# Optimization experiments

Hardware: AMD Instinct MI355X
Metric: run time of the kernel (lower is better)

The kernel has to match this reference:

```python
import jax, jax.numpy as jnp
import numpy as np
from jax import lax

CANTOR_DEPTH = 8
VOCAB, D = 100000, 128


def setup_inputs() -> dict:
    key = jax.random.key(0)
    pentachora = jax.random.normal(key, (VOCAB, 5, D), dtype=jnp.float32)
    return {"pentachora": pentachora}


def _cantor_positions(V):
    # V: [N, 5, D]
    dt = V.dtype
    diff = V[:, :, None, :] - V[:, None, :, :]          # [N,5,5,D]
    dist_sq = jnp.sum(diff * diff, axis=-1)             # [N,5,5]
    N = V.shape[0]

    # Batched 6x6 Cayley-Menger matrix
    M = jnp.zeros((N, 6, 6), dtype=dt)
    M = M.at[:, 0, 1:].set(1.0)
    M = M.at[:, 1:, 0].set(1.0)
    M = M.at[:, 1:, 1:].set(dist_sq)
    det = jnp.linalg.det(M)                              # [N]
    volume = jnp.sqrt(jnp.clip(-det / 9216.0, 0.0))

    # Edge statistics over the 10 unique edges (torch .std() uses ddof=1)
    iu, ju = np.triu_indices(5, k=1)
    edge_lengths = jnp.sqrt(dist_sq[:, iu, ju])          # [N,10]
    mean_edge = jnp.mean(edge_lengths, axis=-1)
    std_edge = jnp.std(edge_lengths, axis=-1, ddof=1)

    # Vertex spread from centroid (ddof=1)
    centroid = jnp.mean(V, axis=1, keepdims=True)        # [N,1,D]
    cdist = jnp.linalg.norm(V - centroid, axis=-1)       # [N,5]
    spread = jnp.std(cdist, axis=-1, ddof=1)

    volume_norm = jax.nn.sigmoid(volume * 10.0)
    edge_ratio = jax.nn.sigmoid(std_edge / (mean_edge + 1e-6))
    spread_norm = jax.nn.sigmoid(spread)

    seed = jnp.clip(volume_norm * 0.4 + edge_ratio * 0.3 + spread_norm * 0.3,
                    1e-6, 1.0 - 1e-6)
    drift = (volume_norm + edge_ratio + spread_norm) * 0.01

    def step(carry, factor):
        x, cv = carry
        x_scaled = x * 3.0
        digit = jnp.floor(x_scaled)                      # x>0 so floor==trunc
        x_frac = x_scaled - digit
        cv = cv + (digit == 2.0).astype(dt) * factor
        x = jnp.clip(x_frac + drift, 1e-6, 1.0 - 1e-6)
        return (x, cv), None

    factors = (0.5 ** jnp.arange(1, CANTOR_DEPTH + 1)).astype(dt)
    (_, cantor_val), _ = lax.scan(step, (seed, jnp.zeros_like(seed)), factors)
    return jnp.clip(cantor_val, 0.0, 1.0)                # [N]


def reference(pentachora):
    return _cantor_positions(pentachora)
```

## Files before the change

### kernel.cpp

```cpp
#include <hip/hip_runtime.h>
#include <math.h>


__global__ __launch_bounds__(256) void fingerprint_kernel(
    const float* __restrict__ pent, float* __restrict__ out, int nItems)
{
    const int tid  = threadIdx.x;
    const int wave = tid >> 6;
    const int lane = tid & 63;
    const int grp  = lane >> 3;
    const int s    = lane & 7;

    long item  = (long)blockIdx.x * 32 + (long)wave * 8 + grp;
    long itemC = item < nItems ? item : (long)nItems - 1;

    const float4* __restrict__ p =
        reinterpret_cast<const float4*>(pent + itemC * 640L);

    float4 f[5][4];
#pragma unroll
    for (int v = 0; v < 5; ++v)
#pragma unroll
        for (int j = 0; j < 4; ++j)
            f[v][j] = p[v * 32 + j * 8 + s];

    const float* fp = reinterpret_cast<const float*>(f);

    double g[15];
#pragma unroll
    for (int q = 0; q < 15; ++q) g[q] = 0.0;

#pragma unroll
    for (int t = 0; t < 16; ++t) {
        double a[5];
#pragma unroll
        for (int v = 0; v < 5; ++v)
            a[v] = (double)fp[v * 16 + t];
        int q = 0;
#pragma unroll
        for (int i = 0; i < 5; ++i)
#pragma unroll
            for (int j = i; j < 5; ++j) {
                g[q] = fma(a[i], a[j], g[q]);
                ++q;
            }
    }

#pragma unroll
    for (int m = 1; m <= 4; m <<= 1)
#pragma unroll
        for (int q = 0; q < 15; ++q) g[q] += __shfl_xor(g[q], m, 64);


    double G[5][5];
    {
        int q = 0;
#pragma unroll
        for (int i = 0; i < 5; ++i)
#pragma unroll
            for (int j = i; j < 5; ++j) {
                G[i][j] = g[q];
                G[j][i] = g[q];
                ++q;
            }
    }

    double S[5], T = 0.0;
#pragma unroll
    for (int i = 0; i < 5; ++i) {
        S[i] = G[i][0] + G[i][1] + G[i][2] + G[i][3] + G[i][4];
        T += S[i];
    }

    double d2[10];
    {
        int q = 0;
#pragma unroll
        for (int i = 0; i < 5; ++i)
#pragma unroll
            for (int j = i + 1; j < 5; ++j) {
                d2[q] = fma(-2.0, G[i][j], G[i][i] + G[j][j]);
                ++q;
            }
    }

    double W[4][4];
#pragma unroll
    for (int pi = 0; pi < 4; ++pi)
#pragma unroll
        for (int qi = 0; qi < 4; ++qi)
            W[pi][qi] = G[pi + 1][qi + 1] - G[0][qi + 1] - G[pi + 1][0] + G[0][0];

    double det = 1.0;
#pragma unroll
    for (int k = 0; k < 4; ++k) {
        double pv = W[k][k];
        det *= pv;
        double inv = (pv != 0.0) ? 1.0 / pv : 0.0;
#pragma unroll
        for (int r = k + 1; r < 4; ++r) {
            double fac = W[r][k] * inv;
#pragma unroll
            for (int c = k + 1; c < 4; ++c)
                W[r][c] = fma(-fac, W[k][c], W[r][c]);
        }
    }

    double v2 = det / 576.0;
    double volume = (v2 > 0.0) ? sqrt(v2) : 0.0;

    double e[10], se = 0.0;
#pragma unroll
    for (int q = 0; q < 10; ++q) { e[q] = sqrt(d2[q]); se += e[q]; }
    double meanE = se * 0.1;
    double ve = 0.0;
#pragma unroll
    for (int q = 0; q < 10; ++q) { double d = e[q] - meanE; ve = fma(d, d, ve); }
    double stdE = sqrt(ve / 9.0);

    double cd[5], scd = 0.0;
#pragma unroll
    for (int v = 0; v < 5; ++v) {
        double c2 = fma(-0.4, S[v], G[v][v]) + 0.04 * T;
        cd[v] = (c2 > 0.0) ? sqrt(c2) : 0.0;
        scd += cd[v];
    }
    double meanC = scd * 0.2;
    double vc = 0.0;
#pragma unroll
    for (int v = 0; v < 5; ++v) { double d = cd[v] - meanC; vc = fma(d, d, vc); }
    double spread = sqrt(vc * 0.25);

    double vn = 1.0 / (1.0 + exp(-10.0 * volume));
    double er = 1.0 / (1.0 + exp(-(stdE / (meanE + 1e-6))));
    double sn = 1.0 / (1.0 + exp(-spread));

    double seed = 0.4 * vn + 0.3 * er + 0.3 * sn;
    seed = fmin(fmax(seed, 1e-6), 1.0 - 1e-6);
    double drift = (vn + er + sn) * 0.01;

    double x = seed, cv = 0.0, factor = 0.5;
#pragma unroll
    for (int k = 0; k < 8; ++k) {
        double xs = x * 3.0;
        double dg = floor(xs);
        double fr = xs - dg;
        cv += (dg == 2.0) ? factor : 0.0;
        factor *= 0.5;
        x = fmin(fmax(fr + drift, 1e-6), 1.0 - 1e-6);
    }
    cv = fmin(fmax(cv, 0.0), 1.0);

    if (s == 0 && item < nItems)
        out[item] = (float)cv;
}

extern "C" void kernel_launch(void* const* d_in, const int* in_sizes, int n_in,
                              void* d_out, int out_size, void* d_ws, size_t ws_size,
                              hipStream_t stream) {
    const float* pent = (const float*)d_in[0];
    float* out = (float*)d_out;
    int nItems = in_sizes[0] / 640;
    int blocks = (nItems + 31) / 32;
    hipLaunchKernelGGL(fingerprint_kernel, dim3(blocks), dim3(256), 0, stream,
                       pent, out, nItems);
}
```

Before: 49.36 us.

## Compact per-item epilogue into one wave via LDS handoff of Gram sums

After the shuffle reduction, each 8-lane group writes its 15 reduced Gram entries to shared memory. The first 32 threads then each run the scalar double-precision epilogue (distances, determinant, sigmoids, Cantor loop) for one item, instead of all 256 lanes computing it redundantly. This cuts the redundant FP64 work to one wave per block, at the cost of a block barrier and LDS traffic. The launch bounds also gain a minimum-blocks hint, which may constrain register allocation.

```diff
diff --git a/kernel.cpp b/kernel.cpp
--- a/kernel.cpp
+++ b/kernel.cpp
@@ -2,9 +2,15 @@
 #include <math.h>
 
 
-__global__ __launch_bounds__(256) void fingerprint_kernel(
+__device__ __forceinline__ constexpr int gidx(int i, int j) {
+    return i * 5 - i * (i - 1) / 2 + (j - i);
+}
+
+__global__ __launch_bounds__(256, 4) void fingerprint_kernel(
     const float* __restrict__ pent, float* __restrict__ out, int nItems)
 {
+    __shared__ double lds_g[32][15];
+
     const int tid  = threadIdx.x;
     const int wave = tid >> 6;
     const int lane = tid & 63;
@@ -51,108 +57,128 @@
 #pragma unroll
         for (int q = 0; q < 15; ++q) g[q] += __shfl_xor(g[q], m, 64);
 
+    if (s == 0) {
+        const int slot = wave * 8 + grp;
+#pragma unroll
+        for (int q = 0; q < 15; ++q) lds_g[slot][q] = g[q];
+    }
+    __syncthreads();
 
-    double G[5][5];
-    {
-        int q = 0;
+    if (tid < 32) {
+        const long item2 = (long)blockIdx.x * 32 + tid;
+
+        double h[15];
 #pragma unroll
-        for (int i = 0; i < 5; ++i)
+        for (int q = 0; q < 15; ++q) h[q] = lds_g[tid][q];
+
+        double e[10];
+        double se = 0.0;
+        {
+            int q = 0;
 #pragma unroll
-            for (int j = i; j < 5; ++j) {
-                G[i][j] = g[q];
-                G[j][i] = g[q];
-                ++q;
+            for (int i = 0; i < 5; ++i)
+#pragma unroll
+                for (int j = i + 1; j < 5; ++j) {
+                    double d2 = fma(-2.0, h[gidx(i, j)],
+                                    h[gidx(i, i)] + h[gidx(j, j)]);
+                    e[q] = sqrt(d2);
+                    se += e[q];
+                    ++q;
+                }
+        }
+        double meanE = se * 0.1;
+        double ve = 0.0;
+#pragma unroll
+        for (int q = 0; q < 10; ++q) {
+            double d = e[q] - meanE;
+            ve = fma(d, d, ve);
+        }
+        double stdE = sqrt(ve / 9.0);
+
+        double S[5], T = 0.0;
+#pragma unroll
+        for (int i = 0; i < 5; ++i) {
+            double si = 0.0;
+#pragma unroll
+            for (int j = 0; j < 5; ++j) {
+                int a = i < j ? i : j;
+                int b = i < j ? j : i;
+                si += h[gidx(a, b)];
             }
+            S[i] = si;
+            T += si;
+        }
+
+        double scd = 0.0, cd[5];
+#pragma unroll
+        for (int v = 0; v < 5; ++v) {
+            double c2 = fma(-0.4, S[v], h[gidx(v, v)]) + 0.04 * T;
+            cd[v] = (c2 > 0.0) ? sqrt(c2) : 0.0;
+            scd += cd[v];
+        }
+        double meanC = scd * 0.2;
+        double vc = 0.0;
+#pragma unroll
+        for (int v = 0; v < 5; ++v) {
+            double d = cd[v] - meanC;
+            vc = fma(d, d, vc);
+        }
+        double spread = sqrt(vc * 0.25);
+
+        double W[4][4];
+#pragma unroll
+        for (int pi = 0; pi < 4; ++pi)
+#pragma unroll
+            for (int qi = 0; qi < 4; ++qi) {
+                int a0 = 0, b0 = qi + 1;
+                int a1 = 0, b1 = pi + 1;
+                int lo = (pi < qi ? pi : qi) + 1;
+                int hi = (pi < qi ? qi : pi) + 1;
+                W[pi][qi] = h[gidx(lo, hi)] - h[gidx(a0, b0)]
+                          - h[gidx(a1, b1)] + h[gidx(0, 0)];
+            }
+
+        double det = 1.0;
+#pragma unroll
+        for (int k = 0; k < 4; ++k) {
+            double pv = W[k][k];
+            det *= pv;
+            double inv = (pv != 0.0) ? 1.0 / pv : 0.0;
+#pragma unroll
+            for (int r = k + 1; r < 4; ++r) {
+                double fac = W[r][k] * inv;
+#pragma unroll
+                for (int c = k + 1; c < 4; ++c)
+                    W[r][c] = fma(-fac, W[k][c], W[r][c]);
+            }
+        }
+
+        double v2 = det / 576.0;
+        double volume = (v2 > 0.0) ? sqrt(v2) : 0.0;
+
+        double vn = 1.0 / (1.0 + exp(-10.0 * volume));
+        double er = 1.0 / (1.0 + exp(-(stdE / (meanE + 1e-6))));
+        double sn = 1.0 / (1.0 + exp(-spread));
+
+        double seed = 0.4 * vn + 0.3 * er + 0.3 * sn;
+        seed = fmin(fmax(seed, 1e-6), 1.0 - 1e-6);
+        double drift = (vn + er + sn) * 0.01;
+
+        double x = seed, cv = 0.0, factor = 0.5;
+#pragma unroll
+        for (int k = 0; k < 8; ++k) {
+            double xs = x * 3.0;
+            double dg = floor(xs);
+            double fr = xs - dg;
+            cv += (dg == 2.0) ? factor : 0.0;
+            factor *= 0.5;
+            x = fmin(fmax(fr + drift, 1e-6), 1.0 - 1e-6);
+        }
+        cv = fmin(fmax(cv, 0.0), 1.0);
+
+        if (item2 < nItems)
+            out[item2] = (float)cv;
     }
-
-    double S[5], T = 0.0;
-#pragma unroll
-    for (int i = 0; i < 5; ++i) {
-        S[i] = G[i][0] + G[i][1] + G[i][2] + G[i][3] + G[i][4];
-        T += S[i];
-    }
-
-    double d2[10];
-    {
-        int q = 0;
-#pragma unroll
-        for (int i = 0; i < 5; ++i)
-#pragma unroll
-            for (int j = i + 1; j < 5; ++j) {
-                d2[q] = fma(-2.0, G[i][j], G[i][i] + G[j][j]);
-                ++q;
-            }
-    }
-
-    double W[4][4];
-#pragma unroll
-    for (int pi = 0; pi < 4; ++pi)
-#pragma unroll
-        for (int qi = 0; qi < 4; ++qi)
-            W[pi][qi] = G[pi + 1][qi + 1] - G[0][qi + 1] - G[pi + 1][0] + G[0][0];
-
-    double det = 1.0;
-#pragma unroll
-    for (int k = 0; k < 4; ++k) {
-        double pv = W[k][k];
-        det *= pv;
-        double inv = (pv != 0.0) ? 1.0 / pv : 0.0;
-#pragma unroll
-        for (int r = k + 1; r < 4; ++r) {
-            double fac = W[r][k] * inv;
-#pragma unroll
-            for (int c = k + 1; c < 4; ++c)
-                W[r][c] = fma(-fac, W[k][c], W[r][c]);
-        }
-    }
-
-    double v2 = det / 576.0;
-    double volume = (v2 > 0.0) ? sqrt(v2) : 0.0;
-
-    double e[10], se = 0.0;
-#pragma unroll
-    for (int q = 0; q < 10; ++q) { e[q] = sqrt(d2[q]); se += e[q]; }
-    double meanE = se * 0.1;
-    double ve = 0.0;
-#pragma unroll
-    for (int q = 0; q < 10; ++q) { double d = e[q] - meanE; ve = fma(d, d, ve); }
-    double stdE = sqrt(ve / 9.0);
-
-    double cd[5], scd = 0.0;
-#pragma unroll
-    for (int v = 0; v < 5; ++v) {
-        double c2 = fma(-0.4, S[v], G[v][v]) + 0.04 * T;
-        cd[v] = (c2 > 0.0) ? sqrt(c2) : 0.0;
-        scd += cd[v];
-    }
-    double meanC = scd * 0.2;
-    double vc = 0.0;
-#pragma unroll
-    for (int v = 0; v < 5; ++v) { double d = cd[v] - meanC; vc = fma(d, d, vc); }
-    double spread = sqrt(vc * 0.25);
-
-    double vn = 1.0 / (1.0 + exp(-10.0 * volume));
-    double er = 1.0 / (1.0 + exp(-(stdE / (meanE + 1e-6))));
-    double sn = 1.0 / (1.0 + exp(-spread));
-
-    double seed = 0.4 * vn + 0.3 * er + 0.3 * sn;
-    seed = fmin(fmax(seed, 1e-6), 1.0 - 1e-6);
-    double drift = (vn + er + sn) * 0.01;
-
-    double x = seed, cv = 0.0, factor = 0.5;
-#pragma unroll
-    for (int k = 0; k < 8; ++k) {
-        double xs = x * 3.0;
-        double dg = floor(xs);
-        double fr = xs - dg;
-        cv += (dg == 2.0) ? factor : 0.0;
-        factor *= 0.5;
-        x = fmin(fmax(fr + drift, 1e-6), 1.0 - 1e-6);
-    }
-    cv = fmin(fmax(cv, 0.0), 1.0);
-
-    if (s == 0 && item < nItems)
-        out[item] = (float)cv;
 }
 
 extern "C" void kernel_launch(void* const* d_in, const int* in_sizes, int n_in,
```

Result: faster. 45.11 us (-8.6%).
